# Performance work log

Measured on AMD Instinct MI355X. Metric: run time of the kernel, lower is better.

## Reference

```python
import jax, jax.numpy as jnp
import numpy as np

B = 2
H = W = 128
N = H * W            # 16384 nodes
K_LOC = 7 * 7        # 49 local neighbors (KxK unfold window)
K_LONG = int(K_LOC * 0.2)  # 9 long-range random neighbors
KT = K_LOC + K_LONG  # 58 total neighbors per node
D = 64               # prop_dim
EPS = 1e-12


def setup_inputs() -> dict:
    key = jax.random.key(0)
    k1, k2, k3 = jax.random.split(key, 3)
    logits = jax.random.normal(k1, (B, N, KT), dtype=jnp.float32)
    h0 = jax.random.normal(k2, (B, N, D), dtype=jnp.float32)
    v_inds = jax.random.randint(k3, (B, N, KT), 0, N)  # neighbor (column) indices
    return {"logits": logits, "h0": h0, "v_inds": v_inds, "num_iters": 10}


def reference(logits, h0, v_inds, num_iters):
    """Core of SymbolicGrouper.extract_segments:
    - local adjacency: softmax over K then max-normalize per row
    - scatter into (transposed) sparse global affinity: A[v, u] = adj[u, k], v = v_inds[u, k]
    - graph propagation: h <- normalize(A @ h), iterated.
    """
    Bn, Nn, Kt = logits.shape
    # local adjacency: softmax + max-normalize (matches extract_segments)
    adj = jax.nn.softmax(logits, axis=-1)
    adj = adj / jnp.clip(jnp.max(adj, axis=-1, keepdims=True), EPS, None)
    # validity mask (col_inds < N in local_to_sparse_global_affinity)
    adj = jnp.where(v_inds < Nn, adj, jnp.zeros((), adj.dtype))
    # h0 initialized as softmax of normal noise
    h = jax.nn.softmax(h0, axis=-1)

    def prop_one(adj_b, v_b, h_b):
        v_flat = v_b.reshape(-1)  # [N*K]

        def step(hc, _):
            # message from source node u along each of its K edges: [N, K, D]
            contrib = adj_b[:, :, None] * hc[:, None, :]
            # transposed scatter: accumulate into destination v (A^T semantics)
            out = jnp.zeros_like(hc).at[v_flat].add(contrib.reshape(-1, hc.shape[-1]))
            # per-node L2 renormalization keeps propagation stable
            out = out / jnp.clip(jnp.linalg.norm(out, axis=-1, keepdims=True), EPS, None)
            return out, None

        h_final, _ = jax.lax.scan(step, h_b, None, length=num_iters)
        return h_final

    return jax.vmap(prop_one)(adj, v_inds, h)  # [B, N, D]
```

## Files before the change

kernel.cpp:

```cpp
#include <hip/hip_runtime.h>
#include <hip/hip_fp16.h>

#define B_ 2
#define N_ 16384
#define KT_ 58
#define D_ 64
#define BN_ (B_ * N_)
#define EDGES_ (B_ * N_ * KT_)
#define NUM_ITERS_ 10
#define EPS_ 1e-12f
#define CAP_ 128
#define NPART_ 8
#define FBLK_ 256
#define CHUNK_ (EDGES_ / FBLK_)

__global__ __launch_bounds__(256) void k_adj(const float* __restrict__ logits,
                                             unsigned int* __restrict__ rec_src) {
    const int lane = threadIdx.x & 63;
    const int r = blockIdx.x * 4 + (threadIdx.x >> 6);
    float l = (lane < KT_) ? logits[(size_t)r * KT_ + lane] : -INFINITY;
    float m = l;
    #pragma unroll
    for (int off = 32; off; off >>= 1) m = fmaxf(m, __shfl_xor(m, off));
    if (lane < KT_) {
        float w = __expf(l - m);
        unsigned int wb = (unsigned int)__half_as_ushort(__float2half_rn(w));
        rec_src[(size_t)r * KT_ + lane] = (wb << 16) | (unsigned int)r;
    }
}

__global__ __launch_bounds__(256) void k_fillx(const int* __restrict__ v_inds,
                                               const unsigned int* __restrict__ rec_src,
                                               int* __restrict__ cursor,
                                               unsigned int* __restrict__ bucket) {
    const int part = blockIdx.x & (NPART_ - 1);
    const int m = blockIdx.x >> 3;
    const int t = threadIdx.x;
    const int base = m * CHUNK_;
    #pragma unroll 4
    for (int i = 0; i < CHUNK_ / 256; ++i) {
        const int e = base + i * 256 + t;
        const int v = __builtin_nontemporal_load(v_inds + e);
        const unsigned int rec = __builtin_nontemporal_load(rec_src + e);
        if (v < N_) {
            const int b = (e >= N_ * KT_) ? 1 : 0;
            const int gv = (b << 14) + v;
            if ((gv >> 12) == part) {
                const int pos = atomicAdd(&cursor[gv], 1);
                if (pos < CAP_) bucket[(size_t)gv * CAP_ + pos] = rec;
            }
        }
    }
}

__global__ __launch_bounds__(256) void k_hinit(const float* __restrict__ h0,
                                               __half* __restrict__ h) {
    const int lane = threadIdx.x & 63;
    const int r = blockIdx.x * 4 + (threadIdx.x >> 6);
    float x = h0[(size_t)r * D_ + lane];
    float m = x;
    #pragma unroll
    for (int off = 32; off; off >>= 1) m = fmaxf(m, __shfl_xor(m, off));
    float ex = __expf(x - m);
    float s = ex;
    #pragma unroll
    for (int off = 32; off; off >>= 1) s += __shfl_xor(s, off);
    h[(size_t)r * D_ + lane] = __float2half_rn(ex / s);
}

template <bool FINAL>
__global__ __launch_bounds__(256) void k_prop(const int* __restrict__ cursor,
                                              const unsigned int* __restrict__ bucket,
                                              const __half* __restrict__ h_in,
                                              __half* __restrict__ h_out,
                                              float* __restrict__ out_f) {
    const int lane = threadIdx.x & 63;
    const int grp = lane >> 3;
    const int j = lane & 7;
    const int p = blockIdx.x & 7;
    const int m = blockIdx.x >> 3;
    const int wid = threadIdx.x >> 6;
    int g;
    if (p < 4) g = ((m * 4 + p) << 2) + wid;
    else       g = N_ + ((m * 4 + (p - 4)) << 2) + wid;
    g = __builtin_amdgcn_readfirstlane(g);

    const int cnt = min(cursor[g], CAP_);
    const unsigned int* brow = bucket + (size_t)g * CAP_;
    const unsigned int r0 = __builtin_nontemporal_load(brow + lane);
    const unsigned int r1 = (cnt > 64)
        ? __builtin_nontemporal_load(brow + 64 + lane) : 0u;
    const uint4* __restrict__ h4 = (const uint4*)h_in;

    float a0 = 0.f, a1 = 0.f, a2 = 0.f, a3 = 0.f;
    float a4 = 0.f, a5 = 0.f, a6 = 0.f, a7 = 0.f;
    const int c0 = min(cnt, 64);
    #pragma unroll 2
    for (int e0 = 0; e0 < c0; e0 += 8) {
        const int e = e0 + grp;
        unsigned int rec = __shfl(r0, e);
        rec = (e < cnt) ? rec : 0u;
        const float w = __half2float(__ushort_as_half((unsigned short)(rec >> 16)));
        const int u = (int)(rec & 0xffffu);
        const uint4 x = h4[(size_t)u * 8 + j];
        const __half2 p0 = *(const __half2*)&x.x;
        const __half2 p1 = *(const __half2*)&x.y;
        const __half2 p2 = *(const __half2*)&x.z;
        const __half2 p3 = *(const __half2*)&x.w;
        a0 = fmaf(__half2float(__low2half(p0)), w, a0);
        a1 = fmaf(__half2float(__high2half(p0)), w, a1);
        a2 = fmaf(__half2float(__low2half(p1)), w, a2);
        a3 = fmaf(__half2float(__high2half(p1)), w, a3);
        a4 = fmaf(__half2float(__low2half(p2)), w, a4);
        a5 = fmaf(__half2float(__high2half(p2)), w, a5);
        a6 = fmaf(__half2float(__low2half(p3)), w, a6);
        a7 = fmaf(__half2float(__high2half(p3)), w, a7);
    }
    if (cnt > 64) {
        #pragma unroll 2
        for (int e0 = 64; e0 < cnt; e0 += 8) {
            const int e = e0 + grp;
            unsigned int rec = __shfl(r1, e & 63);
            rec = (e < cnt) ? rec : 0u;
            const float w = __half2float(__ushort_as_half((unsigned short)(rec >> 16)));
            const int u = (int)(rec & 0xffffu);
            const uint4 x = h4[(size_t)u * 8 + j];
            const __half2 p0 = *(const __half2*)&x.x;
            const __half2 p1 = *(const __half2*)&x.y;
            const __half2 p2 = *(const __half2*)&x.z;
            const __half2 p3 = *(const __half2*)&x.w;
            a0 = fmaf(__half2float(__low2half(p0)), w, a0);
            a1 = fmaf(__half2float(__high2half(p0)), w, a1);
            a2 = fmaf(__half2float(__low2half(p1)), w, a2);
            a3 = fmaf(__half2float(__high2half(p1)), w, a3);
            a4 = fmaf(__half2float(__low2half(p2)), w, a4);
            a5 = fmaf(__half2float(__high2half(p2)), w, a5);
            a6 = fmaf(__half2float(__low2half(p3)), w, a6);
            a7 = fmaf(__half2float(__high2half(p3)), w, a7);
        }
    }

    #pragma unroll
    for (int off = 8; off <= 32; off <<= 1) {
        a0 += __shfl_xor(a0, off); a1 += __shfl_xor(a1, off);
        a2 += __shfl_xor(a2, off); a3 += __shfl_xor(a3, off);
        a4 += __shfl_xor(a4, off); a5 += __shfl_xor(a5, off);
        a6 += __shfl_xor(a6, off); a7 += __shfl_xor(a7, off);
    }

    float n2 = a0 * a0 + a1 * a1 + a2 * a2 + a3 * a3 +
               a4 * a4 + a5 * a5 + a6 * a6 + a7 * a7;
    #pragma unroll
    for (int off = 4; off; off >>= 1) n2 += __shfl_xor(n2, off);
    const float inv = 1.0f / fmaxf(sqrtf(n2), EPS_);

    if (grp == 0) {
        if (FINAL) {
            float4* o = (float4*)out_f + (size_t)g * 16 + j * 2;
            o[0] = make_float4(a0 * inv, a1 * inv, a2 * inv, a3 * inv);
            o[1] = make_float4(a4 * inv, a5 * inv, a6 * inv, a7 * inv);
        } else {
            __half2 q0 = __floats2half2_rn(a0 * inv, a1 * inv);
            __half2 q1 = __floats2half2_rn(a2 * inv, a3 * inv);
            __half2 q2 = __floats2half2_rn(a4 * inv, a5 * inv);
            __half2 q3 = __floats2half2_rn(a6 * inv, a7 * inv);
            uint4 o;
            o.x = *(const unsigned int*)&q0;
            o.y = *(const unsigned int*)&q1;
            o.z = *(const unsigned int*)&q2;
            o.w = *(const unsigned int*)&q3;
            ((uint4*)h_out)[(size_t)g * 8 + j] = o;
        }
    }
}

extern "C" void kernel_launch(void* const* d_in, const int* in_sizes, int n_in,
                              void* d_out, int out_size, void* d_ws, size_t ws_size,
                              hipStream_t stream) {
    const float* logits = (const float*)d_in[0];
    const float* h0 = (const float*)d_in[1];
    const int* v_inds = (const int*)d_in[2];
    float* out = (float*)d_out;

    char* ws = (char*)d_ws;
    size_t off = 0;
    auto alloc = [&](size_t bytes) {
        void* p = ws + off;
        off = (off + bytes + 255) & ~(size_t)255;
        return p;
    };
    unsigned int* rec_src = (unsigned int*)alloc((size_t)EDGES_ * 4);
    unsigned int* bucket  = (unsigned int*)alloc((size_t)BN_ * CAP_ * 4);
    int* cursor   = (int*)alloc((size_t)BN_ * 4);
    __half* h_a   = (__half*)alloc((size_t)BN_ * D_ * 2);
    __half* h_b   = (__half*)alloc((size_t)BN_ * D_ * 2);

    hipMemsetAsync(cursor, 0, (size_t)BN_ * 4, stream);

    k_adj<<<BN_ / 4, 256, 0, stream>>>(logits, rec_src);
    k_hinit<<<BN_ / 4, 256, 0, stream>>>(h0, h_a);
    k_fillx<<<NPART_ * FBLK_, 256, 0, stream>>>(v_inds, rec_src, cursor, bucket);

    const __half* cur = h_a;
    for (int i = 0; i < NUM_ITERS_; ++i) {
        __half* nxt = (i & 1) ? h_a : h_b;
        if (i == NUM_ITERS_ - 1) {
            k_prop<true><<<BN_ / 4, 256, 0, stream>>>(cursor, bucket, cur, nullptr, out);
        } else {
            k_prop<false><<<BN_ / 4, 256, 0, stream>>>(cursor, bucket, cur, nxt, nullptr);
        }
        cur = nxt;
    }
}
```

Baseline: 385.2 us.

## Process two destination nodes per wave and pack neighbor index with weight

Each wave in the propagation kernel now handles two adjacent destination rows, interleaving their gathers to raise memory-level parallelism and halving the grid. The first 64 edge slots are always iterated with masking instead of a count-bounded loop. The adjacency kernel now reads v_inds and packs weight plus destination index, so the fill kernel reads one array instead of two and recovers the source from the edge index via a division. This raises register pressure and may waste gather work on padded slots. The bucket-row loads also change from nontemporal to ordinary loads.

```diff
diff --git a/kernel.cpp b/kernel.cpp
--- a/kernel.cpp
+++ b/kernel.cpp
@@ -15,7 +15,8 @@
 #define CHUNK_ (EDGES_ / FBLK_)
 
 __global__ __launch_bounds__(256) void k_adj(const float* __restrict__ logits,
-                                             unsigned int* __restrict__ rec_src) {
+                                             const int* __restrict__ v_inds,
+                                             unsigned int* __restrict__ packed) {
     const int lane = threadIdx.x & 63;
     const int r = blockIdx.x * 4 + (threadIdx.x >> 6);
     float l = (lane < KT_) ? logits[(size_t)r * KT_ + lane] : -INFINITY;
@@ -23,14 +24,15 @@
     #pragma unroll
     for (int off = 32; off; off >>= 1) m = fmaxf(m, __shfl_xor(m, off));
     if (lane < KT_) {
-        float w = __expf(l - m);
+        const int v = v_inds[(size_t)r * KT_ + lane];
+        float w = (v < N_) ? __expf(l - m) : 0.f;
         unsigned int wb = (unsigned int)__half_as_ushort(__float2half_rn(w));
-        rec_src[(size_t)r * KT_ + lane] = (wb << 16) | (unsigned int)r;
-    }
-}
-
-__global__ __launch_bounds__(256) void k_fillx(const int* __restrict__ v_inds,
-                                               const unsigned int* __restrict__ rec_src,
+        unsigned int vv = (v < N_) ? (unsigned int)v : 0u;
+        packed[(size_t)r * KT_ + lane] = (wb << 16) | vv;
+    }
+}
+
+__global__ __launch_bounds__(256) void k_fillx(const unsigned int* __restrict__ packed,
                                                int* __restrict__ cursor,
                                                unsigned int* __restrict__ bucket) {
     const int part = blockIdx.x & (NPART_ - 1);
@@ -40,15 +42,13 @@
     #pragma unroll 4
     for (int i = 0; i < CHUNK_ / 256; ++i) {
         const int e = base + i * 256 + t;
-        const int v = __builtin_nontemporal_load(v_inds + e);
-        const unsigned int rec = __builtin_nontemporal_load(rec_src + e);
-        if (v < N_) {
-            const int b = (e >= N_ * KT_) ? 1 : 0;
-            const int gv = (b << 14) + v;
-            if ((gv >> 12) == part) {
-                const int pos = atomicAdd(&cursor[gv], 1);
-                if (pos < CAP_) bucket[(size_t)gv * CAP_ + pos] = rec;
-            }
+        const unsigned int pk = __builtin_nontemporal_load(packed + e);
+        const int v = (int)(pk & 0x3fffu);
+        const int gv = ((e >= N_ * KT_) ? N_ : 0) + v;
+        if ((gv >> 12) == part) {
+            const unsigned int u = (unsigned int)(e / KT_);
+            const int pos = atomicAdd(&cursor[gv], 1);
+            if (pos < CAP_) bucket[(size_t)gv * CAP_ + pos] = (pk & 0xffff0000u) | u;
         }
     }
 }
@@ -67,6 +67,26 @@
     for (int off = 32; off; off >>= 1) s += __shfl_xor(s, off);
     h[(size_t)r * D_ + lane] = __float2half_rn(ex / s);
 }
+
+#define PROC_EDGE(REC, A0, A1, A2, A3, A4, A5, A6, A7)                        \
+    {                                                                          \
+        const float w =                                                        \
+            __half2float(__ushort_as_half((unsigned short)((REC) >> 16)));     \
+        const int u = (int)((REC) & 0xffffu);                                  \
+        const uint4 x = h4[(size_t)u * 8 + j];                                 \
+        const __half2 p0 = *(const __half2*)&x.x;                              \
+        const __half2 p1 = *(const __half2*)&x.y;                              \
+        const __half2 p2 = *(const __half2*)&x.z;                              \
+        const __half2 p3 = *(const __half2*)&x.w;                              \
+        A0 = fmaf(__half2float(__low2half(p0)), w, A0);                        \
+        A1 = fmaf(__half2float(__high2half(p0)), w, A1);                       \
+        A2 = fmaf(__half2float(__low2half(p1)), w, A2);                        \
+        A3 = fmaf(__half2float(__high2half(p1)), w, A3);                       \
+        A4 = fmaf(__half2float(__low2half(p2)), w, A4);                        \
+        A5 = fmaf(__half2float(__high2half(p2)), w, A5);                       \
+        A6 = fmaf(__half2float(__low2half(p3)), w, A6);                        \
+        A7 = fmaf(__half2float(__high2half(p3)), w, A7);                       \
+    }
 
 template <bool FINAL>
 __global__ __launch_bounds__(256) void k_prop(const int* __restrict__ cursor,
@@ -80,63 +100,49 @@
     const int p = blockIdx.x & 7;
     const int m = blockIdx.x >> 3;
     const int wid = threadIdx.x >> 6;
-    int g;
-    if (p < 4) g = ((m * 4 + p) << 2) + wid;
-    else       g = N_ + ((m * 4 + (p - 4)) << 2) + wid;
-    g = __builtin_amdgcn_readfirstlane(g);
-
-    const int cnt = min(cursor[g], CAP_);
-    const unsigned int* brow = bucket + (size_t)g * CAP_;
-    const unsigned int r0 = __builtin_nontemporal_load(brow + lane);
-    const unsigned int r1 = (cnt > 64)
-        ? __builtin_nontemporal_load(brow + 64 + lane) : 0u;
+    int g0 = (p << 12) + (((m << 2) + wid) << 1);
+    g0 = __builtin_amdgcn_readfirstlane(g0);
+    const int g1 = g0 + 1;
+
+    const int cntA = min(cursor[g0], CAP_);
+    const int cntB = min(cursor[g1], CAP_);
+    const unsigned int* browA = bucket + (size_t)g0 * CAP_;
+    const unsigned int* browB = bucket + (size_t)g1 * CAP_;
+    const unsigned int r0A = browA[lane];
+    const unsigned int r0B = browB[lane];
     const uint4* __restrict__ h4 = (const uint4*)h_in;
 
     float a0 = 0.f, a1 = 0.f, a2 = 0.f, a3 = 0.f;
     float a4 = 0.f, a5 = 0.f, a6 = 0.f, a7 = 0.f;
-    const int c0 = min(cnt, 64);
-    #pragma unroll 2
-    for (int e0 = 0; e0 < c0; e0 += 8) {
+    float b0 = 0.f, b1 = 0.f, b2 = 0.f, b3 = 0.f;
+    float b4 = 0.f, b5 = 0.f, b6 = 0.f, b7 = 0.f;
+
+    #pragma unroll 4
+    for (int e0 = 0; e0 < 64; e0 += 8) {
         const int e = e0 + grp;
-        unsigned int rec = __shfl(r0, e);
-        rec = (e < cnt) ? rec : 0u;
-        const float w = __half2float(__ushort_as_half((unsigned short)(rec >> 16)));
-        const int u = (int)(rec & 0xffffu);
-        const uint4 x = h4[(size_t)u * 8 + j];
-        const __half2 p0 = *(const __half2*)&x.x;
-        const __half2 p1 = *(const __half2*)&x.y;
-        const __half2 p2 = *(const __half2*)&x.z;
-        const __half2 p3 = *(const __half2*)&x.w;
-        a0 = fmaf(__half2float(__low2half(p0)), w, a0);
-        a1 = fmaf(__half2float(__high2half(p0)), w, a1);
-        a2 = fmaf(__half2float(__low2half(p1)), w, a2);
-        a3 = fmaf(__half2float(__high2half(p1)), w, a3);
-        a4 = fmaf(__half2float(__low2half(p2)), w, a4);
-        a5 = fmaf(__half2float(__high2half(p2)), w, a5);
-        a6 = fmaf(__half2float(__low2half(p3)), w, a6);
-        a7 = fmaf(__half2float(__high2half(p3)), w, a7);
-    }
-    if (cnt > 64) {
-        #pragma unroll 2
-        for (int e0 = 64; e0 < cnt; e0 += 8) {
+        unsigned int recA = __shfl(r0A, e);
+        unsigned int recB = __shfl(r0B, e);
+        recA = (e < cntA) ? recA : 0u;
+        recB = (e < cntB) ? recB : 0u;
+        PROC_EDGE(recA, a0, a1, a2, a3, a4, a5, a6, a7)
+        PROC_EDGE(recB, b0, b1, b2, b3, b4, b5, b6, b7)
+    }
+    if (cntA > 64) {
+        const unsigned int r1A = browA[64 + lane];
+        for (int e0 = 64; e0 < cntA; e0 += 8) {
             const int e = e0 + grp;
-            unsigned int rec = __shfl(r1, e & 63);
-            rec = (e < cnt) ? rec : 0u;
-            const float w = __half2float(__ushort_as_half((unsigned short)(rec >> 16)));
-            const int u = (int)(rec & 0xffffu);
-            const uint4 x = h4[(size_t)u * 8 + j];
-            const __half2 p0 = *(const __half2*)&x.x;
-            const __half2 p1 = *(const __half2*)&x.y;
-            const __half2 p2 = *(const __half2*)&x.z;
-            const __half2 p3 = *(const __half2*)&x.w;
-            a0 = fmaf(__half2float(__low2half(p0)), w, a0);
-            a1 = fmaf(__half2float(__high2half(p0)), w, a1);
-            a2 = fmaf(__half2float(__low2half(p1)), w, a2);
-            a3 = fmaf(__half2float(__high2half(p1)), w, a3);
-            a4 = fmaf(__half2float(__low2half(p2)), w, a4);
-            a5 = fmaf(__half2float(__high2half(p2)), w, a5);
-            a6 = fmaf(__half2float(__low2half(p3)), w, a6);
-            a7 = fmaf(__half2float(__high2half(p3)), w, a7);
+            unsigned int rec = __shfl(r1A, e & 63);
+            rec = (e < cntA) ? rec : 0u;
+            PROC_EDGE(rec, a0, a1, a2, a3, a4, a5, a6, a7)
+        }
+    }
+    if (cntB > 64) {
+        const unsigned int r1B = browB[64 + lane];
+        for (int e0 = 64; e0 < cntB; e0 += 8) {
+            const int e = e0 + grp;
+            unsigned int rec = __shfl(r1B, e & 63);
+            rec = (e < cntB) ? rec : 0u;
+            PROC_EDGE(rec, b0, b1, b2, b3, b4, b5, b6, b7)
         }
     }
 
@@ -146,30 +152,53 @@
         a2 += __shfl_xor(a2, off); a3 += __shfl_xor(a3, off);
         a4 += __shfl_xor(a4, off); a5 += __shfl_xor(a5, off);
         a6 += __shfl_xor(a6, off); a7 += __shfl_xor(a7, off);
-    }
-
-    float n2 = a0 * a0 + a1 * a1 + a2 * a2 + a3 * a3 +
+        b0 += __shfl_xor(b0, off); b1 += __shfl_xor(b1, off);
+        b2 += __shfl_xor(b2, off); b3 += __shfl_xor(b3, off);
+        b4 += __shfl_xor(b4, off); b5 += __shfl_xor(b5, off);
+        b6 += __shfl_xor(b6, off); b7 += __shfl_xor(b7, off);
+    }
+
+    float nA = a0 * a0 + a1 * a1 + a2 * a2 + a3 * a3 +
                a4 * a4 + a5 * a5 + a6 * a6 + a7 * a7;
-    #pragma unroll
-    for (int off = 4; off; off >>= 1) n2 += __shfl_xor(n2, off);
-    const float inv = 1.0f / fmaxf(sqrtf(n2), EPS_);
+    float nB = b0 * b0 + b1 * b1 + b2 * b2 + b3 * b3 +
+               b4 * b4 + b5 * b5 + b6 * b6 + b7 * b7;
+    #pragma unroll
+    for (int off = 4; off; off >>= 1) {
+        nA += __shfl_xor(nA, off);
+        nB += __shfl_xor(nB, off);
+    }
+    const float invA = 1.0f / fmaxf(sqrtf(nA), EPS_);
+    const float invB = 1.0f / fmaxf(sqrtf(nB), EPS_);
 
     if (grp == 0) {
         if (FINAL) {
-            float4* o = (float4*)out_f + (size_t)g * 16 + j * 2;
-            o[0] = make_float4(a0 * inv, a1 * inv, a2 * inv, a3 * inv);
-            o[1] = make_float4(a4 * inv, a5 * inv, a6 * inv, a7 * inv);
+            float4* oA = (float4*)out_f + (size_t)g0 * 16 + j * 2;
+            oA[0] = make_float4(a0 * invA, a1 * invA, a2 * invA, a3 * invA);
+            oA[1] = make_float4(a4 * invA, a5 * invA, a6 * invA, a7 * invA);
+            float4* oB = (float4*)out_f + (size_t)g1 * 16 + j * 2;
+            oB[0] = make_float4(b0 * invB, b1 * invB, b2 * invB, b3 * invB);
+            oB[1] = make_float4(b4 * invB, b5 * invB, b6 * invB, b7 * invB);
         } else {
-            __half2 q0 = __floats2half2_rn(a0 * inv, a1 * inv);
-            __half2 q1 = __floats2half2_rn(a2 * inv, a3 * inv);
-            __half2 q2 = __floats2half2_rn(a4 * inv, a5 * inv);
-            __half2 q3 = __floats2half2_rn(a6 * inv, a7 * inv);
-            uint4 o;
-            o.x = *(const unsigned int*)&q0;
-            o.y = *(const unsigned int*)&q1;
-            o.z = *(const unsigned int*)&q2;
-            o.w = *(const unsigned int*)&q3;
-            ((uint4*)h_out)[(size_t)g * 8 + j] = o;
+            __half2 q0 = __floats2half2_rn(a0 * invA, a1 * invA);
+            __half2 q1 = __floats2half2_rn(a2 * invA, a3 * invA);
+            __half2 q2 = __floats2half2_rn(a4 * invA, a5 * invA);
+            __half2 q3 = __floats2half2_rn(a6 * invA, a7 * invA);
+            uint4 oA;
+            oA.x = *(const unsigned int*)&q0;
+            oA.y = *(const unsigned int*)&q1;
+            oA.z = *(const unsigned int*)&q2;
+            oA.w = *(const unsigned int*)&q3;
+            ((uint4*)h_out)[(size_t)g0 * 8 + j] = oA;
+            __half2 s0 = __floats2half2_rn(b0 * invB, b1 * invB);
+            __half2 s1 = __floats2half2_rn(b2 * invB, b3 * invB);
+            __half2 s2 = __floats2half2_rn(b4 * invB, b5 * invB);
+            __half2 s3 = __floats2half2_rn(b6 * invB, b7 * invB);
+            uint4 oB;
+            oB.x = *(const unsigned int*)&s0;
+            oB.y = *(const unsigned int*)&s1;
+            oB.z = *(const unsigned int*)&s2;
+            oB.w = *(const unsigned int*)&s3;
+            ((uint4*)h_out)[(size_t)g1 * 8 + j] = oB;
         }
     }
 }
@@ -189,25 +218,25 @@
         off = (off + bytes + 255) & ~(size_t)255;
         return p;
     };
-    unsigned int* rec_src = (unsigned int*)alloc((size_t)EDGES_ * 4);
-    unsigned int* bucket  = (unsigned int*)alloc((size_t)BN_ * CAP_ * 4);
+    unsigned int* packed = (unsigned int*)alloc((size_t)EDGES_ * 4);
+    unsigned int* bucket = (unsigned int*)alloc((size_t)BN_ * CAP_ * 4);
     int* cursor   = (int*)alloc((size_t)BN_ * 4);
     __half* h_a   = (__half*)alloc((size_t)BN_ * D_ * 2);
     __half* h_b   = (__half*)alloc((size_t)BN_ * D_ * 2);
 
     hipMemsetAsync(cursor, 0, (size_t)BN_ * 4, stream);
 
-    k_adj<<<BN_ / 4, 256, 0, stream>>>(logits, rec_src);
+    k_adj<<<BN_ / 4, 256, 0, stream>>>(logits, v_inds, packed);
     k_hinit<<<BN_ / 4, 256, 0, stream>>>(h0, h_a);
-    k_fillx<<<NPART_ * FBLK_, 256, 0, stream>>>(v_inds, rec_src, cursor, bucket);
+    k_fillx<<<NPART_ * FBLK_, 256, 0, stream>>>(packed, cursor, bucket);
 
     const __half* cur = h_a;
     for (int i = 0; i < NUM_ITERS_; ++i) {
         __half* nxt = (i & 1) ? h_a : h_b;
         if (i == NUM_ITERS_ - 1) {
-            k_prop<true><<<BN_ / 4, 256, 0, stream>>>(cursor, bucket, cur, nullptr, out);
+            k_prop<true><<<BN_ / 8, 256, 0, stream>>>(cursor, bucket, cur, nullptr, out);
         } else {
-            k_prop<false><<<BN_ / 4, 256, 0, stream>>>(cursor, bucket, cur, nxt, nullptr);
+            k_prop<false><<<BN_ / 8, 256, 0, stream>>>(cursor, bucket, cur, nxt, nullptr);
         }
         cur = nxt;
     }
```

After: 381.4 us. No clear change (-1.0%).
